# Performance work log

Measured on AMD Instinct MI355X. Metric: run time of the kernel, lower is better.

Reference implementation:

```python
import jax, jax.numpy as jnp
import numpy as np

N, E, F0, H, ED, C = 50000, 800000, 32, 64, 13, 10
EPS_BN = 1e-5
EPS_STD = 1e-5


def setup_inputs() -> dict:
    keys = iter(jax.random.split(jax.random.key(0), 64))

    def w(shape):
        return jax.random.normal(next(keys), shape, jnp.float32) * 0.05

    inp = {
        "x": jax.random.normal(next(keys), (N, F0), jnp.float32),
        "edge_index": jax.random.randint(next(keys), (2, E), 0, N),
        "edge_attr": jax.random.normal(next(keys), (E, ED), jnp.float32),
    }
    for l, (fi, fo) in enumerate([(F0, H), (H, 2 * H), (2 * H, 4 * H)], 1):
        inp[f"we{l}"] = w((ED, fi));   inp[f"be{l}"] = jnp.zeros((fi,), jnp.float32)   # edge encoder
        inp[f"wp{l}"] = w((3 * fi, fi)); inp[f"bp{l}"] = jnp.zeros((fi,), jnp.float32)  # pre-MLP (1 layer)
        inp[f"wo{l}"] = w((13 * fi, fo)); inp[f"bo{l}"] = jnp.zeros((fo,), jnp.float32) # post-MLP (1 layer)
        inp[f"wl{l}"] = w((fo, fo));   inp[f"bl{l}"] = jnp.zeros((fo,), jnp.float32)   # PNAConv.lin
        inp[f"g{l}"] = jnp.ones((fo,), jnp.float32); inp[f"bb{l}"] = jnp.zeros((fo,), jnp.float32)  # BatchNorm
    inp["wc"] = w((4 * H, C)); inp["bc"] = jnp.zeros((C,), jnp.float32)  # classifier
    return inp


def _pna_conv(x, src, dst, edge_attr, cnt, avg_log, we, be, wp, bp, wo, bo, wl, bl):
    n = x.shape[0]
    e = edge_attr @ we + be                            # [E, F_in] edge encoder
    h = jnp.concatenate([x[dst], x[src], e], -1)       # [E, 3*F_in] = (x_i, x_j, edge)
    m = h @ wp + bp                                    # pre-MLP message, [E, F_in]
    denom = jnp.maximum(cnt, 1.0)[:, None]
    mean = jax.ops.segment_sum(m, dst, n) / denom
    mean2 = jax.ops.segment_sum(m * m, dst, n) / denom
    has = (cnt > 0)[:, None]
    mn = jnp.where(has, jax.ops.segment_min(m, dst, n), 0.0)
    mx = jnp.where(has, jax.ops.segment_max(m, dst, n), 0.0)
    std = jnp.sqrt(jax.nn.relu(mean2 - mean * mean) + EPS_STD)
    agg = jnp.concatenate([mean, mn, mx, std], -1)     # [N, 4*F_in]
    logd = jnp.log(jnp.maximum(cnt, 1.0) + 1.0)[:, None]
    scaled = jnp.concatenate([agg, agg * (logd / avg_log), agg * (avg_log / logd)], -1)  # [N, 12*F_in]
    out = jnp.concatenate([x, scaled], -1) @ wo + bo   # post-MLP on [N, 13*F_in]
    return out @ wl + bl                                # PNAConv.lin


def _bn_relu(x, g, b):
    mu = jnp.mean(x, 0)
    var = jnp.mean((x - mu) ** 2, 0)  # biased, training-mode BatchNorm
    return jax.nn.relu(g * (x - mu) / jnp.sqrt(var + EPS_BN) + b)


def _forward(edge_index, x, edge_attr, *p):
    src, dst = edge_index[0], edge_index[1]
    n = x.shape[0]
    cnt = jax.ops.segment_sum(jnp.ones((edge_index.shape[1],), jnp.float32), dst, n)
    avg_log = jnp.mean(jnp.log(cnt + 1.0))  # PNA avg_deg['log'] from in-degree histogram
    (we1, be1, wp1, bp1, wo1, bo1, wl1, bl1, g1, bb1,
     we2, be2, wp2, bp2, wo2, bo2, wl2, bl2, g2, bb2,
     we3, be3, wp3, bp3, wo3, bo3, wl3, bl3, g3, bb3, wc, bc) = p
    x = _bn_relu(_pna_conv(x, src, dst, edge_attr, cnt, avg_log, we1, be1, wp1, bp1, wo1, bo1, wl1, bl1), g1, bb1)
    x = _bn_relu(_pna_conv(x, src, dst, edge_attr, cnt, avg_log, we2, be2, wp2, bp2, wo2, bo2, wl2, bl2), g2, bb2)
    x = _bn_relu(_pna_conv(x, src, dst, edge_attr, cnt, avg_log, we3, be3, wp3, bp3, wo3, bo3, wl3, bl3), g3, bb3)
    return x @ wc + bc


def reference(x, edge_index, edge_attr,
              we1, be1, wp1, bp1, wo1, bo1, wl1, bl1, g1, bb1,
              we2, be2, wp2, bp2, wo2, bo2, wl2, bl2, g2, bb2,
              we3, be3, wp3, bp3, wo3, bo3, wl3, bl3, g3, bb3,
              wc, bc):
    return _forward(edge_index, x, edge_attr,
                    we1, be1, wp1, bp1, wo1, bo1, wl1, bl1, g1, bb1,
                    we2, be2, wp2, bp2, wo2, bo2, wl2, bl2, g2, bb2,
                    we3, be3, wp3, bp3, wo3, bo3, wl3, bl3, g3, bb3, wc, bc)
```

## Files before the change

### kernel.cpp

```cpp
#include <hip/hip_runtime.h>
#include <math.h>
#include <float.h>

#define NN 50000
#define NE 800000

typedef __attribute__((ext_vector_type(8))) short bf16x8;
typedef __attribute__((ext_vector_type(4))) short bf16x4;
typedef __attribute__((ext_vector_type(2))) short bf16x2;
typedef __attribute__((ext_vector_type(4))) float f32x4;

template<int NC> struct VecT;
template<> struct VecT<2>{ using type = bf16x2; };
template<> struct VecT<4>{ using type = bf16x4; };

__device__ inline short f2bf(float f){
  union { float f; unsigned u; } v; v.f = f;
  unsigned u = v.u + 0x7FFFu + ((v.u >> 16) & 1u);
  return (short)(u >> 16);
}

__device__ inline float bf2f(short b){
  union { unsigned u; float f; } v;
  v.u = ((unsigned)(unsigned short)b) << 16;
  return v.f;
}


__global__ void k_count(const int* __restrict__ dst, int* __restrict__ cnt){
  int e = blockIdx.x*blockDim.x + threadIdx.x;
  if (e < NE) atomicAdd(&cnt[dst[e]], 1);
}

__global__ void k_scan_part(const int* __restrict__ cnt, int* __restrict__ offs, int* __restrict__ totals){
  __shared__ int sh[1024];
  int t = threadIdx.x, i = blockIdx.x*1024 + t;
  int v = (i < NN) ? cnt[i] : 0;
  sh[t] = v; __syncthreads();
  for (int off = 1; off < 1024; off <<= 1){
    int x = (t >= off) ? sh[t-off] : 0;
    __syncthreads();
    sh[t] += x;
    __syncthreads();
  }
  if (i < NN) offs[i] = sh[t] - v;
  if (t == 1023) totals[blockIdx.x] = sh[t];
}

__global__ void k_scan_tops(int* totals, int nb){
  if (threadIdx.x == 0){
    int acc = 0;
    for (int i = 0; i < nb; i++){ int v = totals[i]; totals[i] = acc; acc += v; }
  }
}

__global__ void k_scan_add(int* __restrict__ offs, const int* __restrict__ totals, int* __restrict__ cursor){
  int i = blockIdx.x*blockDim.x + threadIdx.x;
  if (i < NN){
    int v = offs[i] + totals[i >> 10];
    offs[i] = v;
    cursor[i] = v;
  } else if (i == NN){
    offs[NN] = NE;
  }
}

__global__ void k_scatter(const int* __restrict__ ei, int* __restrict__ cursor,
                          int* __restrict__ ssrc, int* __restrict__ seid){
  int e = blockIdx.x*blockDim.x + threadIdx.x;
  if (e >= NE) return;
  int d = ei[NE + e];
  int p = atomicAdd(&cursor[d], 1);
  ssrc[p] = ei[e];
  seid[p] = e;
}

__global__ void k_permute_ea(const float* __restrict__ ea, const int* __restrict__ seid,
                             short* __restrict__ ea_s){
  int i = blockIdx.x*blockDim.x + threadIdx.x;
  if (i >= NE*16) return;
  int p = i >> 4, r = i & 15;
  int eid = seid[p];
  float v = (r < 13) ? ea[(size_t)eid*13 + r] : ((r == 13) ? 1.0f : 0.f);
  ea_s[i] = f2bf(v);
}

__global__ void k_sumlog(const int* __restrict__ cnt, float* __restrict__ sumlog){
  __shared__ float sh[256];
  int t = threadIdx.x;
  float s = 0.f;
  for (int i = blockIdx.x*256 + t; i < NN; i += gridDim.x*256)
    s += logf((float)cnt[i] + 1.f);
  sh[t] = s; __syncthreads();
  for (int o = 128; o > 0; o >>= 1){ if (t < o) sh[t] += sh[t+o]; __syncthreads(); }
  if (t == 0) atomicAdd(sumlog, sh[0]);
}

__global__ void k_rscale(const int* __restrict__ cnt, const float* __restrict__ sumlog,
                         float* __restrict__ r1, float* __restrict__ r2){
  int i = blockIdx.x*blockDim.x + threadIdx.x;
  if (i >= NN) return;
  float avg = sumlog[0] / (float)NN;
  float logd = logf(fmaxf((float)cnt[i], 1.f) + 1.f);
  r1[i] = logd / avg;
  r2[i] = avg / logd;
}

__global__ void k_f2bf_arr(const float* __restrict__ in, short* __restrict__ out, int n){
  int i = blockIdx.x*blockDim.x + threadIdx.x;
  if (i < n) out[i] = f2bf(in[i]);
}

__global__ void k_prep_wcT(const float* __restrict__ wc, short* __restrict__ wcT){
  int idx = blockIdx.x*blockDim.x + threadIdx.x;
  if (idx >= 2560) return;
  int c = idx >> 8, k = idx & 255;
  wcT[idx] = f2bf(wc[k*10 + c]);
}

__global__ __launch_bounds__(256) void k_prep_wol(int K13, int fo,
    const float* __restrict__ wo, const float* __restrict__ wl,
    short* __restrict__ WolT)
{
  __shared__ short As[64*40];
  __shared__ short Bs[64*40];
  int tid = threadIdx.x;
  int lane = tid & 63, w = tid >> 6;
  int wr = w >> 1, wc = w & 1;
  int l15 = lane & 15, l16 = lane >> 4;
  int row0 = blockIdx.x*64, col0 = blockIdx.y*64;
  int sr = tid >> 2, sq = tid & 3;
  f32x4 acc[2][2] = {};
  for (int k0 = 0; k0 < fo; k0 += 32){
    int gr = row0 + sr;
    bf16x8 av = {0,0,0,0,0,0,0,0};
    if (gr < K13){
      const float4* src = (const float4*)(wo + (size_t)gr*fo + k0 + sq*8);
      float4 f0 = src[0], f1 = src[1];
      av[0]=f2bf(f0.x); av[1]=f2bf(f0.y); av[2]=f2bf(f0.z); av[3]=f2bf(f0.w);
      av[4]=f2bf(f1.x); av[5]=f2bf(f1.y); av[6]=f2bf(f1.z); av[7]=f2bf(f1.w);
    }
    *(bf16x8*)&As[sr*40 + sq*8] = av;
    int gc = col0 + sr;
    bf16x8 bv;
    #pragma unroll
    for (int e = 0; e < 8; e++)
      bv[e] = f2bf(wl[(size_t)(k0 + sq*8 + e)*fo + gc]);
    *(bf16x8*)&Bs[sr*40 + sq*8] = bv;
    __syncthreads();
    bf16x8 af[2], bg[2];
    #pragma unroll
    for (int m = 0; m < 2; m++) af[m] = *(bf16x8*)&As[(wr*32 + m*16 + l15)*40 + l16*8];
    #pragma unroll
    for (int n = 0; n < 2; n++) bg[n] = *(bf16x8*)&Bs[(wc*32 + n*16 + l15)*40 + l16*8];
    #pragma unroll
    for (int m = 0; m < 2; m++)
      #pragma unroll
      for (int n = 0; n < 2; n++)
        acc[m][n] = __builtin_amdgcn_mfma_f32_16x16x32_bf16(af[m], bg[n], acc[m][n], 0, 0, 0);
    __syncthreads();
  }
  #pragma unroll
  for (int m = 0; m < 2; m++){
    #pragma unroll
    for (int n = 0; n < 2; n++){
      int gcol = col0 + wc*32 + n*16 + l15;
      int grow0 = row0 + wr*32 + m*16 + l16*4;
      if (grow0 < K13){
        bf16x4 ov;
        #pragma unroll
        for (int i = 0; i < 4; i++) ov[i] = f2bf(acc[m][n][i]);
        *(bf16x4*)(WolT + (size_t)gcol*K13 + grow0) = ov;
      }
    }
  }
}

__global__ void k_prep_layer(const float* __restrict__ we, const float* __restrict__ be,
                             const float* __restrict__ wp, const float* __restrict__ bp,
                             short* __restrict__ WeLT, float* __restrict__ bL2,
                             short* __restrict__ wpT,
                             float* __restrict__ bns, int fi, int NCW){
  int fo = 2*fi;
  int n0 = fi*32;
  int n1 = n0 + 2*fi;
  int n2 = n1 + 2*fi*fi;
  int n3 = n2 + 2*fo;
  int idx = blockIdx.x*blockDim.x + threadIdx.x;
  if (idx < n0){
    int jg = idx >> 5, k = idx & 31;
    int Wd = NCW*16;
    int sub = jg / Wd, j = jg - sub*Wd;
    int f = sub*Wd + NCW*(j & 15) + (j >> 4);
    float s = 0.f;
    if (k < 13){
      const float* wpb = wp + (size_t)2*fi*fi;
      const float* wr = we + k*fi;
      for (int jj = 0; jj < fi; jj++) s += wr[jj] * wpb[(size_t)jj*fi + f];
    }
    WeLT[idx] = f2bf(s);
  } else if (idx < n1){
    int f = idx - n0;
    if (f >= fi){ bL2[f] = 0.f; }
    else {
      const float* wpb = wp + (size_t)2*fi*fi;
      float s = bp[f];
      for (int j = 0; j < fi; j++) s += be[j] * wpb[(size_t)j*fi + f];
      bL2[f] = s;
    }
  } else if (idx < n2){
    int id = idx - n1;
    int s = id/(fi*fi), rem = id - s*fi*fi;
    int f = rem/fi, j = rem - f*fi;
    wpT[id] = f2bf(wp[((size_t)s*fi + j)*fi + f]);
  } else if (idx < n3){
    bns[idx - n2] = 0.f;
  }
}

__global__ __launch_bounds__(256) void k_gemm_t(int M, int Nout, int K,
    const short* __restrict__ A, const short* __restrict__ BT,
    const float* __restrict__ bias, short* __restrict__ Cb)
{
  __shared__ short As[64*40];
  __shared__ short Bs[64*40];
  int tid = threadIdx.x;
  int lane = tid & 63, w = tid >> 6;
  int wr = w >> 1, wc = w & 1;
  int l15 = lane & 15, l16 = lane >> 4;
  int row0 = blockIdx.x*64, col0 = blockIdx.y*64;
  int sr = tid >> 2, sq = tid & 3;
  f32x4 acc[2][2] = {};
  for (int k0 = 0; k0 < K; k0 += 32){
    int gr = row0 + sr;
    bf16x8 av = {0,0,0,0,0,0,0,0};
    if (gr < M) av = *(const bf16x8*)(A + (size_t)gr*K + k0 + sq*8);
    *(bf16x8*)&As[sr*40 + sq*8] = av;
    int gc = col0 + sr;
    bf16x8 bv = {0,0,0,0,0,0,0,0};
    if (gc < Nout) bv = *(const bf16x8*)(BT + (size_t)gc*K + k0 + sq*8);
    *(bf16x8*)&Bs[sr*40 + sq*8] = bv;
    __syncthreads();
    bf16x8 af[2], bg[2];
    #pragma unroll
    for (int m = 0; m < 2; m++) af[m] = *(bf16x8*)&As[(wr*32 + m*16 + l15)*40 + l16*8];
    #pragma unroll
    for (int n = 0; n < 2; n++) bg[n] = *(bf16x8*)&Bs[(wc*32 + n*16 + l15)*40 + l16*8];
    #pragma unroll
    for (int m = 0; m < 2; m++)
      #pragma unroll
      for (int n = 0; n < 2; n++)
        acc[m][n] = __builtin_amdgcn_mfma_f32_16x16x32_bf16(af[m], bg[n], acc[m][n], 0, 0, 0);
    __syncthreads();
  }
  #pragma unroll
  for (int m = 0; m < 2; m++){
    #pragma unroll
    for (int n = 0; n < 2; n++){
      int gcol = col0 + wc*32 + n*16 + l15;
      #pragma unroll
      for (int i = 0; i < 4; i++){
        int grow = row0 + wr*32 + m*16 + l16*4 + i;
        if (grow < M && gcol < Nout)
          Cb[(size_t)grow*Nout + gcol] = f2bf(acc[m][n][i] + (bias ? bias[gcol] : 0.f));
      }
    }
  }
}

__global__ __launch_bounds__(256) void k_mfma(int M, int Nout, int K,
    const short* __restrict__ A,
    const short* __restrict__ BT, int ldbt,
    float* __restrict__ C, int ldc, const float* __restrict__ bias)
{
  __shared__ short As[64*40];
  __shared__ short Bs[64*40];
  int tid = threadIdx.x;
  int lane = tid & 63, w = tid >> 6;
  int wr = w >> 1, wc = w & 1;
  int l15 = lane & 15, l16 = lane >> 4;
  int row0 = blockIdx.x*64, col0 = blockIdx.y*64;
  int sr = tid >> 2, sq = tid & 3;
  f32x4 acc[2][2] = {};
  for (int k0 = 0; k0 < K; k0 += 32){
    int gr = row0 + sr;
    bf16x8 av = {0,0,0,0,0,0,0,0};
    if (gr < M) av = *(const bf16x8*)(A + (size_t)gr*K + k0 + sq*8);
    *(bf16x8*)&As[sr*40 + sq*8] = av;
    int gc = col0 + sr;
    bf16x8 bv = {0,0,0,0,0,0,0,0};
    if (gc < Nout)
      bv = *(const bf16x8*)(BT + (size_t)gc*ldbt + k0 + sq*8);
    *(bf16x8*)&Bs[sr*40 + sq*8] = bv;
    __syncthreads();
    bf16x8 af[2], bg[2];
    #pragma unroll
    for (int m = 0; m < 2; m++) af[m] = *(bf16x8*)&As[(wr*32 + m*16 + l15)*40 + l16*8];
    #pragma unroll
    for (int n = 0; n < 2; n++) bg[n] = *(bf16x8*)&Bs[(wc*32 + n*16 + l15)*40 + l16*8];
    #pragma unroll
    for (int m = 0; m < 2; m++)
      #pragma unroll
      for (int n = 0; n < 2; n++)
        acc[m][n] = __builtin_amdgcn_mfma_f32_16x16x32_bf16(af[m], bg[n], acc[m][n], 0, 0, 0);
    __syncthreads();
  }
  #pragma unroll
  for (int m = 0; m < 2; m++){
    #pragma unroll
    for (int n = 0; n < 2; n++){
      int gcol = col0 + wc*32 + n*16 + l15;
      #pragma unroll
      for (int i = 0; i < 4; i++){
        int grow = row0 + wr*32 + m*16 + l16*4 + i;
        if (grow < M && gcol < Nout)
          C[(size_t)grow*ldc + gcol] = acc[m][n][i] + (bias ? bias[gcol] : 0.f);
      }
    }
  }
}

template<int MREP, int WCG>
__global__ __launch_bounds__(512) void k_mfma_big(int M, int K, int FI,
    const short* __restrict__ P0, const short* __restrict__ P1,
    const short* __restrict__ P2, const short* __restrict__ P3,
    const short* __restrict__ P4,
    const float* __restrict__ r1, const float* __restrict__ r2,
    const short* __restrict__ BT,
    short* __restrict__ Cb, float* __restrict__ bns)
{
  constexpr int NOUT = WCG*64;
  constexpr int ROWS = (8/WCG)*MREP*16;
  constexpr int NR = 8/WCG;
  __shared__ short As[2][ROWS*40];
  __shared__ short Bs[2][NOUT*40];
  const short* Pt[5] = {P0, P1, P2, P3, P4};
  int tid = threadIdx.x;
  int lane = tid & 63, w = tid >> 6;
  int wid_c = w % WCG, wid_r = w / WCG;
  int wrow = wid_r * (MREP*16);
  int wcol = wid_c * 64;
  int l15 = lane & 15, l16 = lane >> 4;
  int row0 = blockIdx.x*ROWS;
  int trowA = tid >> 2, tsegA = tid & 3;
  int trowB = tid >> 1, tsegB = tid & 1;
  int gr = row0 + trowA;
  bool aval = gr < M;
  bool bval = trowB < NOUT;
  const short* bsrc = BT + (size_t)trowB*K + tsegB*16;
  f32x4 acc[MREP][4] = {};
  int nt = K/32;

  bf16x8 a0 = {0,0,0,0,0,0,0,0}, b0 = a0, b1 = a0;
  float sval = 1.f; int smv = 0;

  auto LOAD = [&](int t){
    int k0 = t*32;
    int kb = k0 / FI;
    int pi = (kb == 0) ? 0 : ((kb - 1) & 3) + 1;
    smv = (kb == 0) ? 0 : ((kb - 1) >> 2);
    const short* __restrict__ P = Pt[pi];
    int j0 = k0 - kb*FI + tsegA*8;
    bf16x8 z = {0,0,0,0,0,0,0,0};
    a0 = z; b0 = z; b1 = z;
    sval = 1.f;
    if (aval){
      a0 = *(const bf16x8*)(P + (size_t)gr*FI + j0);
      if (smv) sval = (smv == 1) ? r1[gr] : r2[gr];
    }
    if (bval){
      const bf16x8* src = (const bf16x8*)(bsrc + k0);
      b0 = src[0]; b1 = src[1];
    }
  };

  LOAD(0);
  int cur = 0;
  for (int t = 0; t < nt; t++){
    if (smv && aval){
      #pragma unroll
      for (int e = 0; e < 8; e++) a0[e] = f2bf(bf2f(a0[e])*sval);
    }
    *(bf16x8*)&As[cur][trowA*40 + tsegA*8] = a0;
    if (bval){
      *(bf16x8*)&Bs[cur][trowB*40 + tsegB*16]     = b0;
      *(bf16x8*)&Bs[cur][trowB*40 + tsegB*16 + 8] = b1;
    }
    __syncthreads();
    if (t + 1 < nt) LOAD(t + 1);
    bf16x8 af[MREP], bg[4];
    #pragma unroll
    for (int m = 0; m < MREP; m++) af[m] = *(bf16x8*)&As[cur][(wrow + m*16 + l15)*40 + l16*8];
    #pragma unroll
    for (int n = 0; n < 4; n++) bg[n] = *(bf16x8*)&Bs[cur][(wcol + n*16 + l15)*40 + l16*8];
    #pragma unroll
    for (int m = 0; m < MREP; m++)
      #pragma unroll
      for (int n = 0; n < 4; n++)
        acc[m][n] = __builtin_amdgcn_mfma_f32_16x16x32_bf16(af[m], bg[n], acc[m][n], 0, 0, 0);
    cur ^= 1;
  }
  float ws[4], ws2[4];
  #pragma unroll
  for (int n = 0; n < 4; n++){
    int gcol = wcol + n*16 + l15;
    float s = 0.f, s2 = 0.f;
    #pragma unroll
    for (int m = 0; m < MREP; m++)
      #pragma unroll
      for (int i = 0; i < 4; i++){
        float v = acc[m][n][i];
        s += v; s2 = fmaf(v, v, s2);
        int grow = row0 + wrow + m*16 + l16*4 + i;
        if (grow < M) Cb[(size_t)grow*NOUT + gcol] = f2bf(v);
      }
    s  += __shfl_xor(s, 16, 64);  s  += __shfl_xor(s, 32, 64);
    s2 += __shfl_xor(s2, 16, 64); s2 += __shfl_xor(s2, 32, 64);
    ws[n] = s; ws2[n] = s2;
  }
  float* red = (float*)&As[0][0];
  __syncthreads();
  if (l16 == 0){
    #pragma unroll
    for (int n = 0; n < 4; n++){
      red[w*128 + n*16 + l15]      = ws[n];
      red[w*128 + 64 + n*16 + l15] = ws2[n];
    }
  }
  __syncthreads();
  if (wid_r == 0 && l16 == 0){
    #pragma unroll
    for (int n = 0; n < 4; n++){
      float ts = 0.f, ts2 = 0.f;
      #pragma unroll
      for (int r = 0; r < NR; r++){
        int ww = r*WCG + wid_c;
        ts  += red[ww*128 + n*16 + l15];
        ts2 += red[ww*128 + 64 + n*16 + l15];
      }
      int gcol = wcol + n*16 + l15;
      atomicAdd(&bns[gcol], ts);
      atomicAdd(&bns[NOUT + gcol], ts2);
    }
  }
}

template<int NC, int FI>
__global__ __launch_bounds__(256) void k_agg3(
    const int* __restrict__ offs, const int* __restrict__ ssrc,
    const short* __restrict__ ea_s,
    const short* __restrict__ T,
    const short* __restrict__ WeLT,
    short* __restrict__ mean, short* __restrict__ mn,
    short* __restrict__ mx,  short* __restrict__ stdv)
{
  constexpr int SUBS = FI / (NC*16);
  constexpr int STR = 2*FI;
  using bf16xN = typename VecT<NC>::type;
  const short* t_s = T + FI;
  int wv = (blockIdx.x*blockDim.x + threadIdx.x) >> 6;
  int n = wv / SUBS, sub = wv - n*SUBS;
  if (n >= NN) return;
  int lane = threadIdx.x & 63;
  int l15 = lane & 15, l16 = lane >> 4;
  int c0 = sub * NC * 16;
  bool ins = (l16 == 1);
  bf16xN tdv = *(const bf16xN*)(T + (size_t)n*STR + c0 + NC*l15);
  bf16x8 bfrag[NC];
  #pragma unroll
  for (int c = 0; c < NC; c++){
    bfrag[c] = *(const bf16x8*)(WeLT + (size_t)(c0 + c*16 + l15)*32 + l16*8);
    if (ins) bfrag[c][5] = tdv[c];
  }
  float s[NC], s2[NC], vmn[NC], vmx[NC];
  #pragma unroll
  for (int c = 0; c < NC; c++){ s[c]=0.f; s2[c]=0.f; vmn[c]=FLT_MAX; vmx[c]=-FLT_MAX; }
  int e0 = offs[n], e1 = offs[n+1];
  int p0 = e0;
  int tsoff = c0 + NC*l15;
  for (; p0 + 16 <= e1; p0 += 16){
    bf16x8 afrag = *(const bf16x8*)(ea_s + (size_t)(p0 + l15)*16 + l16*8);
    bf16xN tsv[4];
    #pragma unroll
    for (int i = 0; i < 4; i++){
      int src = ssrc[p0 + l16*4 + i];
      tsv[i] = *(const bf16xN*)(t_s + (size_t)src*STR + tsoff);
    }
    #pragma unroll
    for (int c = 0; c < NC; c++){
      f32x4 acc = {0.f,0.f,0.f,0.f};
      acc = __builtin_amdgcn_mfma_f32_16x16x32_bf16(afrag, bfrag[c], acc, 0, 0, 0);
      #pragma unroll
      for (int i = 0; i < 4; i++){
        float m = acc[i] + bf2f(tsv[i][c]);
        s[c] += m;
        s2[c] = fmaf(m, m, s2[c]);
        vmn[c] = fminf(vmn[c], m);
        vmx[c] = fmaxf(vmx[c], m);
      }
    }
  }
  if (p0 < e1){
    int pa = p0 + l15; if (pa > e1-1) pa = e1-1;
    bf16x8 afrag = *(const bf16x8*)(ea_s + (size_t)pa*16 + l16*8);
    bf16xN tsv[4]; bool val[4];
    #pragma unroll
    for (int i = 0; i < 4; i++){
      int pp = p0 + l16*4 + i;
      val[i] = pp < e1;
      int pc = val[i] ? pp : (e1-1);
      int src = ssrc[pc];
      tsv[i] = *(const bf16xN*)(t_s + (size_t)src*STR + tsoff);
    }
    #pragma unroll
    for (int c = 0; c < NC; c++){
      f32x4 acc = {0.f,0.f,0.f,0.f};
      acc = __builtin_amdgcn_mfma_f32_16x16x32_bf16(afrag, bfrag[c], acc, 0, 0, 0);
      #pragma unroll
      for (int i = 0; i < 4; i++){
        float m = acc[i] + bf2f(tsv[i][c]);
        float mv = val[i] ? m : 0.f;
        s[c] += mv;
        s2[c] = fmaf(mv, mv, s2[c]);
        vmn[c] = fminf(vmn[c], val[i] ? m :  FLT_MAX);
        vmx[c] = fmaxf(vmx[c], val[i] ? m : -FLT_MAX);
      }
    }
  }
  int cdeg = e1 - e0;
  float denom = fmaxf((float)cdeg, 1.f);
  float rden = 1.0f / denom;
  short* outp = (l16==0) ? mean : (l16==1) ? mn : (l16==2) ? mx : stdv;
  bf16xN ov;
  #pragma unroll
  for (int c = 0; c < NC; c++){
    float sv = s[c];   sv  += __shfl_xor(sv, 16, 64);  sv  += __shfl_xor(sv, 32, 64);
    float s2v = s2[c]; s2v += __shfl_xor(s2v, 16, 64); s2v += __shfl_xor(s2v, 32, 64);
    float mnv = vmn[c]; mnv = fminf(mnv, __shfl_xor(mnv, 16, 64)); mnv = fminf(mnv, __shfl_xor(mnv, 32, 64));
    float mxv = vmx[c]; mxv = fmaxf(mxv, __shfl_xor(mxv, 16, 64)); mxv = fmaxf(mxv, __shfl_xor(mxv, 32, 64));
    float me = sv*rden, me2 = s2v*rden;
    float sd = sqrtf(fmaxf(me2 - me*me, 0.f) + 1e-5f);
    float val = (l16==0) ? me : (l16==1) ? (cdeg>0 ? mnv : 0.f)
              : (l16==2) ? (cdeg>0 ? mxv : 0.f) : sd;
    ov[c] = f2bf(val);
  }
  *(bf16xN*)(outp + (size_t)n*FI + c0 + NC*l15) = ov;
}

__global__ void k_bn_apply(const short* __restrict__ x, const float* __restrict__ sums,
                           const float* __restrict__ g, const float* __restrict__ b,
                           short* __restrict__ xbf, int fo, int total){
  int i = blockIdx.x*blockDim.x + threadIdx.x;
  if (i >= total) return;
  int col = i % fo;
  float mu = sums[col] / (float)NN;
  float var = sums[fo + col] / (float)NN - mu*mu;
  float v = (bf2f(x[i]) - mu) * rsqrtf(var + 1e-5f) * g[col] + b[col];
  xbf[i] = f2bf(fmaxf(v, 0.f));
}

extern "C" void kernel_launch(void* const* d_in, const int* in_sizes, int n_in,
                              void* d_out, int out_size, void* d_ws, size_t ws_size,
                              hipStream_t stream){
  const float* x0 = (const float*)d_in[0];
  const int*   ei = (const int*)d_in[1];
  const float* ea = (const float*)d_in[2];
  const float* W[35];
  for (int i = 0; i < 35; i++) W[i] = (const float*)d_in[i];
  const float* wc = W[33];
  const float* bc = W[34];

  char* w = (char*)d_ws;
  auto alloc = [&](size_t bytes)->void*{
    void* p = (void*)w; w += (bytes + 255) & ~(size_t)255; return p;
  };
  int* cnt    = (int*)alloc((size_t)NN*4);
  int* offs   = (int*)alloc((size_t)(NN+1)*4);
  int* cursor = (int*)alloc((size_t)NN*4);
  int* totals = (int*)alloc(64*4);
  int* ssrc   = (int*)alloc((size_t)NE*4);
  int* seid   = (int*)alloc((size_t)NE*4);
  float* sumlog = (float*)alloc(256);
  float* r1   = (float*)alloc((size_t)NN*4);
  float* r2   = (float*)alloc((size_t)NN*4);
  float* bns  = (float*)alloc(512*4);
  float* bL2  = (float*)alloc(256*4);
  short* WeLT = (short*)alloc((size_t)128*32*2);
  short* WolT = (short*)alloc((size_t)256*1664*2);
  short* wpT  = (short*)alloc((size_t)2*128*128*2);
  short* wcT  = (short*)alloc((size_t)10*256*2);
  short* ea_s = (short*)alloc((size_t)(NE+16)*16*2);
  short* agg[4];
  for (int a = 0; a < 4; a++) agg[a] = (short*)alloc((size_t)NN*128*2);
  short* F    = (short*)alloc((size_t)NN*256*2);
  short* xbfA = (short*)alloc((size_t)NN*128*2);
  short* xbfB = (short*)alloc((size_t)NN*256*2);

  hipMemsetAsync(cnt, 0, (size_t)NN*4, stream);
  hipMemsetAsync(sumlog, 0, 4, stream);
  k_count<<<(NE+255)/256, 256, 0, stream>>>(ei + NE, cnt);
  k_scan_part<<<49, 1024, 0, stream>>>(cnt, offs, totals);
  k_scan_tops<<<1, 64, 0, stream>>>(totals, 49);
  k_scan_add<<<(NN+256)/256, 256, 0, stream>>>(offs, totals, cursor);
  k_scatter<<<(NE+255)/256, 256, 0, stream>>>(ei, cursor, ssrc, seid);
  k_permute_ea<<<(NE*16+255)/256, 256, 0, stream>>>(ea, seid, ea_s);
  k_sumlog<<<256, 256, 0, stream>>>(cnt, sumlog);
  k_rscale<<<(NN+255)/256, 256, 0, stream>>>(cnt, sumlog, r1, r2);
  k_prep_wcT<<<10, 256, 0, stream>>>(wc, wcT);
  k_f2bf_arr<<<(NN*32+255)/256, 256, 0, stream>>>(x0, xbfA, NN*32);

  const short* xin = xbfA;
  const int fis[3] = {32, 64, 128};
  const int ncws[3] = {2, 4, 4};
  const int GX = (NN + 63) / 64;
  const int GB2 = (NN + 127) / 128;
  for (int l = 0; l < 3; l++){
    int fi = fis[l], fo = 2*fi;
    const float* we = W[3+10*l+0], *be = W[3+10*l+1];
    const float* wp = W[3+10*l+2], *bp = W[3+10*l+3];
    const float* wo = W[3+10*l+4];
    const float* wl = W[3+10*l+6];
    const float* g  = W[3+10*l+8], *bb = W[3+10*l+9];

    short* T = F;

    int K13 = 13*fi;
    dim3 gw((K13 + 63)/64, fo/64);
    k_prep_wol<<<gw, 256, 0, stream>>>(K13, fo, wo, wl, WolT);

    int nprep = fi*32 + 2*fi + 2*fi*fi + 2*fo;
    k_prep_layer<<<(nprep+255)/256, 256, 0, stream>>>(we, be, wp, bp,
        WeLT, bL2, wpT, bns, fi, ncws[l]);

    dim3 gt(GX, (2*fi) / 64);
    k_gemm_t<<<gt, 256, 0, stream>>>(NN, 2*fi, fi, xin, wpT, bL2, T);

    if (l == 0){
      int GA3 = (NN*64 + 255)/256;
      k_agg3<2,32><<<GA3, 256, 0, stream>>>(offs, ssrc, ea_s, T, WeLT,
          agg[0], agg[1], agg[2], agg[3]);
    } else if (l == 1){
      int GA3 = (NN*64 + 255)/256;
      k_agg3<4,64><<<GA3, 256, 0, stream>>>(offs, ssrc, ea_s, T, WeLT,
          agg[0], agg[1], agg[2], agg[3]);
    } else {
      int GA3 = (NN*2*64 + 255)/256;
      k_agg3<4,128><<<GA3, 256, 0, stream>>>(offs, ssrc, ea_s, T, WeLT,
          agg[0], agg[1], agg[2], agg[3]);
    }

    if (l == 0)
      k_mfma_big<1,1><<<GB2, 512, 0, stream>>>(NN, 13*fi, fi, xin, agg[0], agg[1], agg[2], agg[3],
          r1, r2, WolT, F, bns);
    else if (l == 1)
      k_mfma_big<2,2><<<GB2, 512, 0, stream>>>(NN, 13*fi, fi, xin, agg[0], agg[1], agg[2], agg[3],
          r1, r2, WolT, F, bns);
    else
      k_mfma_big<4,4><<<GB2, 512, 0, stream>>>(NN, 13*fi, fi, xin, agg[0], agg[1], agg[2], agg[3],
          r1, r2, WolT, F, bns);

    short* xbf_next = (l == 0) ? xbfB : ((l == 1) ? xbfA : xbfB);
    k_bn_apply<<<((NN*fo)+255)/256, 256, 0, stream>>>(F, bns, g, bb, xbf_next, fo, NN*fo);

    xin = xbf_next;
  }

  dim3 gc(GX, 1);
  k_mfma<<<gc, 256, 0, stream>>>(NN, 10, 256, xin, wcT, 256, (float*)d_out, 10, bc);
}
```

Before: 605.5 us.

## Fuse BatchNorm+ReLU into next layer's GEMM operand loads and vectorize edge-attr permute

Removes the standalone BN-apply pass by computing per-channel scale/shift coefficients in a tiny kernel and applying BN+ReLU on the fly when the next layer's GEMMs (and the classifier) load their A operand. Ping-pong F buffers replace the separate bf16 activation buffers. The edge-attribute permute now handles one edge per thread with vectorized 16-byte stores, and the aggregation drops redundant min/max masking. The cost is that BN is recomputed in several consumer kernels (gemm_t, mfma_big x-segment, classifier), which adds ALU work and extra loads of bnc to each of them.

```diff
diff --git a/kernel.cpp b/kernel.cpp
--- a/kernel.cpp
+++ b/kernel.cpp
@@ -77,12 +77,18 @@
 
 __global__ void k_permute_ea(const float* __restrict__ ea, const int* __restrict__ seid,
                              short* __restrict__ ea_s){
-  int i = blockIdx.x*blockDim.x + threadIdx.x;
-  if (i >= NE*16) return;
-  int p = i >> 4, r = i & 15;
+  int p = blockIdx.x*blockDim.x + threadIdx.x;
+  if (p >= NE) return;
   int eid = seid[p];
-  float v = (r < 13) ? ea[(size_t)eid*13 + r] : ((r == 13) ? 1.0f : 0.f);
-  ea_s[i] = f2bf(v);
+  const float* src = ea + (size_t)eid*13;
+  short out[16];
+  #pragma unroll
+  for (int r = 0; r < 13; r++) out[r] = f2bf(src[r]);
+  out[13] = (short)0x3F80;
+  out[14] = 0; out[15] = 0;
+  bf16x8* dst = (bf16x8*)(ea_s + (size_t)p*16);
+  dst[0] = *(bf16x8*)&out[0];
+  dst[1] = *(bf16x8*)&out[8];
 }
 
 __global__ void k_sumlog(const int* __restrict__ cnt, float* __restrict__ sumlog){
@@ -116,6 +122,17 @@
   if (idx >= 2560) return;
   int c = idx >> 8, k = idx & 255;
   wcT[idx] = f2bf(wc[k*10 + c]);
+}
+
+__global__ void k_bn_coef(const float* __restrict__ bns, const float* __restrict__ g,
+                          const float* __restrict__ b, float* __restrict__ bnc, int fo){
+  int c = threadIdx.x;
+  if (c >= fo) return;
+  float mu = bns[c] / (float)NN;
+  float var = bns[fo + c] / (float)NN - mu*mu;
+  float sc = g[c] * rsqrtf(var + 1e-5f);
+  bnc[c] = sc;
+  bnc[256 + c] = b[c] - mu*sc;
 }
 
 __global__ __launch_bounds__(256) void k_prep_wol(int K13, int fo,
@@ -220,7 +237,8 @@
 
 __global__ __launch_bounds__(256) void k_gemm_t(int M, int Nout, int K,
     const short* __restrict__ A, const short* __restrict__ BT,
-    const float* __restrict__ bias, short* __restrict__ Cb)
+    const float* __restrict__ bias, short* __restrict__ Cb,
+    const float* __restrict__ bnc)
 {
   __shared__ short As[64*40];
   __shared__ short Bs[64*40];
@@ -234,7 +252,17 @@
   for (int k0 = 0; k0 < K; k0 += 32){
     int gr = row0 + sr;
     bf16x8 av = {0,0,0,0,0,0,0,0};
-    if (gr < M) av = *(const bf16x8*)(A + (size_t)gr*K + k0 + sq*8);
+    if (gr < M){
+      av = *(const bf16x8*)(A + (size_t)gr*K + k0 + sq*8);
+      if (bnc){
+        int cb = k0 + sq*8;
+        #pragma unroll
+        for (int e = 0; e < 8; e++){
+          float v = fmaf(bf2f(av[e]), bnc[cb + e], bnc[256 + cb + e]);
+          av[e] = f2bf(fmaxf(v, 0.f));
+        }
+      }
+    }
     *(bf16x8*)&As[sr*40 + sq*8] = av;
     int gc = col0 + sr;
     bf16x8 bv = {0,0,0,0,0,0,0,0};
@@ -271,7 +299,8 @@
 __global__ __launch_bounds__(256) void k_mfma(int M, int Nout, int K,
     const short* __restrict__ A,
     const short* __restrict__ BT, int ldbt,
-    float* __restrict__ C, int ldc, const float* __restrict__ bias)
+    float* __restrict__ C, int ldc, const float* __restrict__ bias,
+    const float* __restrict__ bnc)
 {
   __shared__ short As[64*40];
   __shared__ short Bs[64*40];
@@ -285,7 +314,17 @@
   for (int k0 = 0; k0 < K; k0 += 32){
     int gr = row0 + sr;
     bf16x8 av = {0,0,0,0,0,0,0,0};
-    if (gr < M) av = *(const bf16x8*)(A + (size_t)gr*K + k0 + sq*8);
+    if (gr < M){
+      av = *(const bf16x8*)(A + (size_t)gr*K + k0 + sq*8);
+      if (bnc){
+        int cb = k0 + sq*8;
+        #pragma unroll
+        for (int e = 0; e < 8; e++){
+          float v = fmaf(bf2f(av[e]), bnc[cb + e], bnc[256 + cb + e]);
+          av[e] = f2bf(fmaxf(v, 0.f));
+        }
+      }
+    }
     *(bf16x8*)&As[sr*40 + sq*8] = av;
     int gc = col0 + sr;
     bf16x8 bv = {0,0,0,0,0,0,0,0};
@@ -327,7 +366,8 @@
     const short* __restrict__ P4,
     const float* __restrict__ r1, const float* __restrict__ r2,
     const short* __restrict__ BT,
-    short* __restrict__ Cb, float* __restrict__ bns)
+    short* __restrict__ Cb, float* __restrict__ bns,
+    const float* __restrict__ bnc)
 {
   constexpr int NOUT = WCG*64;
   constexpr int ROWS = (8/WCG)*MREP*16;
@@ -352,13 +392,14 @@
   int nt = K/32;
 
   bf16x8 a0 = {0,0,0,0,0,0,0,0}, b0 = a0, b1 = a0;
-  float sval = 1.f; int smv = 0;
+  float sval = 1.f; int smv = 0; int bnk = 0;
 
   auto LOAD = [&](int t){
     int k0 = t*32;
     int kb = k0 / FI;
     int pi = (kb == 0) ? 0 : ((kb - 1) & 3) + 1;
     smv = (kb == 0) ? 0 : ((kb - 1) >> 2);
+    bnk = (kb == 0) ? 1 : 0;
     const short* __restrict__ P = Pt[pi];
     int j0 = k0 - kb*FI + tsegA*8;
     bf16x8 z = {0,0,0,0,0,0,0,0};
@@ -367,6 +408,13 @@
     if (aval){
       a0 = *(const bf16x8*)(P + (size_t)gr*FI + j0);
       if (smv) sval = (smv == 1) ? r1[gr] : r2[gr];
+      if (bnk && bnc){
+        #pragma unroll
+        for (int e = 0; e < 8; e++){
+          float v = fmaf(bf2f(a0[e]), bnc[j0 + e], bnc[256 + j0 + e]);
+          a0[e] = f2bf(fmaxf(v, 0.f));
+        }
+      }
     }
     if (bval){
       const bf16x8* src = (const bf16x8*)(bsrc + k0);
@@ -509,8 +557,7 @@
       int pp = p0 + l16*4 + i;
       val[i] = pp < e1;
       int pc = val[i] ? pp : (e1-1);
-      int src = ssrc[pc];
-      tsv[i] = *(const bf16xN*)(t_s + (size_t)src*STR + tsoff);
+      tsv[i] = *(const bf16xN*)(t_s + (size_t)ssrc[pc]*STR + tsoff);
     }
     #pragma unroll
     for (int c = 0; c < NC; c++){
@@ -522,8 +569,8 @@
         float mv = val[i] ? m : 0.f;
         s[c] += mv;
         s2[c] = fmaf(mv, mv, s2[c]);
-        vmn[c] = fminf(vmn[c], val[i] ? m :  FLT_MAX);
-        vmx[c] = fmaxf(vmx[c], val[i] ? m : -FLT_MAX);
+        vmn[c] = fminf(vmn[c], m);
+        vmx[c] = fmaxf(vmx[c], m);
       }
     }
   }
@@ -547,18 +594,6 @@
   *(bf16xN*)(outp + (size_t)n*FI + c0 + NC*l15) = ov;
 }
 
-__global__ void k_bn_apply(const short* __restrict__ x, const float* __restrict__ sums,
-                           const float* __restrict__ g, const float* __restrict__ b,
-                           short* __restrict__ xbf, int fo, int total){
-  int i = blockIdx.x*blockDim.x + threadIdx.x;
-  if (i >= total) return;
-  int col = i % fo;
-  float mu = sums[col] / (float)NN;
-  float var = sums[fo + col] / (float)NN - mu*mu;
-  float v = (bf2f(x[i]) - mu) * rsqrtf(var + 1e-5f) * g[col] + b[col];
-  xbf[i] = f2bf(fmaxf(v, 0.f));
-}
-
 extern "C" void kernel_launch(void* const* d_in, const int* in_sizes, int n_in,
                               void* d_out, int out_size, void* d_ws, size_t ws_size,
                               hipStream_t stream){
@@ -584,6 +619,7 @@
   float* r1   = (float*)alloc((size_t)NN*4);
   float* r2   = (float*)alloc((size_t)NN*4);
   float* bns  = (float*)alloc(512*4);
+  float* bnc  = (float*)alloc(3*512*4);
   float* bL2  = (float*)alloc(256*4);
   short* WeLT = (short*)alloc((size_t)128*32*2);
   short* WolT = (short*)alloc((size_t)256*1664*2);
@@ -592,9 +628,9 @@
   short* ea_s = (short*)alloc((size_t)(NE+16)*16*2);
   short* agg[4];
   for (int a = 0; a < 4; a++) agg[a] = (short*)alloc((size_t)NN*128*2);
-  short* F    = (short*)alloc((size_t)NN*256*2);
+  short* FA   = (short*)alloc((size_t)NN*256*2);
+  short* FB   = (short*)alloc((size_t)NN*256*2);
   short* xbfA = (short*)alloc((size_t)NN*128*2);
-  short* xbfB = (short*)alloc((size_t)NN*256*2);
 
   hipMemsetAsync(cnt, 0, (size_t)NN*4, stream);
   hipMemsetAsync(sumlog, 0, 4, stream);
@@ -603,13 +639,14 @@
   k_scan_tops<<<1, 64, 0, stream>>>(totals, 49);
   k_scan_add<<<(NN+256)/256, 256, 0, stream>>>(offs, totals, cursor);
   k_scatter<<<(NE+255)/256, 256, 0, stream>>>(ei, cursor, ssrc, seid);
-  k_permute_ea<<<(NE*16+255)/256, 256, 0, stream>>>(ea, seid, ea_s);
+  k_permute_ea<<<(NE+255)/256, 256, 0, stream>>>(ea, seid, ea_s);
   k_sumlog<<<256, 256, 0, stream>>>(cnt, sumlog);
   k_rscale<<<(NN+255)/256, 256, 0, stream>>>(cnt, sumlog, r1, r2);
   k_prep_wcT<<<10, 256, 0, stream>>>(wc, wcT);
   k_f2bf_arr<<<(NN*32+255)/256, 256, 0, stream>>>(x0, xbfA, NN*32);
 
-  const short* xin = xbfA;
+  const short* act = xbfA;
+  const float* actBN = nullptr;
   const int fis[3] = {32, 64, 128};
   const int ncws[3] = {2, 4, 4};
   const int GX = (NN + 63) / 64;
@@ -622,7 +659,8 @@
     const float* wl = W[3+10*l+6];
     const float* g  = W[3+10*l+8], *bb = W[3+10*l+9];
 
-    short* T = F;
+    short* Fcur = (l & 1) ? FB : FA;
+    short* T = Fcur;
 
     int K13 = 13*fi;
     dim3 gw((K13 + 63)/64, fo/64);
@@ -633,7 +671,7 @@
         WeLT, bL2, wpT, bns, fi, ncws[l]);
 
     dim3 gt(GX, (2*fi) / 64);
-    k_gemm_t<<<gt, 256, 0, stream>>>(NN, 2*fi, fi, xin, wpT, bL2, T);
+    k_gemm_t<<<gt, 256, 0, stream>>>(NN, 2*fi, fi, act, wpT, bL2, T, actBN);
 
     if (l == 0){
       int GA3 = (NN*64 + 255)/256;
@@ -650,21 +688,21 @@
     }
 
     if (l == 0)
-      k_mfma_big<1,1><<<GB2, 512, 0, stream>>>(NN, 13*fi, fi, xin, agg[0], agg[1], agg[2], agg[3],
-          r1, r2, WolT, F, bns);
+      k_mfma_big<1,1><<<GB2, 512, 0, stream>>>(NN, 13*fi, fi, act, agg[0], agg[1], agg[2], agg[3],
+          r1, r2, WolT, Fcur, bns, actBN);
     else if (l == 1)
-      k_mfma_big<2,2><<<GB2, 512, 0, stream>>>(NN, 13*fi, fi, xin, agg[0], agg[1], agg[2], agg[3],
-          r1, r2, WolT, F, bns);
+      k_mfma_big<2,2><<<GB2, 512, 0, stream>>>(NN, 13*fi, fi, act, agg[0], agg[1], agg[2], agg[3],
+          r1, r2, WolT, Fcur, bns, actBN);
     else
-      k_mfma_big<4,4><<<GB2, 512, 0, stream>>>(NN, 13*fi, fi, xin, agg[0], agg[1], agg[2], agg[3],
-          r1, r2, WolT, F, bns);
-
-    short* xbf_next = (l == 0) ? xbfB : ((l == 1) ? xbfA : xbfB);
-    k_bn_apply<<<((NN*fo)+255)/256, 256, 0, stream>>>(F, bns, g, bb, xbf_next, fo, NN*fo);
-
-    xin = xbf_next;
+      k_mfma_big<4,4><<<GB2, 512, 0, stream>>>(NN, 13*fi, fi, act, agg[0], agg[1], agg[2], agg[3],
+          r1, r2, WolT, Fcur, bns, actBN);
+
+    k_bn_coef<<<1, 256, 0, stream>>>(bns, g, bb, bnc + l*512, fo);
+
+    act = Fcur;
+    actBN = bnc + l*512;
   }
 
   dim3 gc(GX, 1);
-  k_mfma<<<gc, 256, 0, stream>>>(NN, 10, 256, xin, wcT, 256, (float*)d_out, 10, bc);
-}
+  k_mfma<<<gc, 256, 0, stream>>>(NN, 10, 256, act, wcT, 256, (float*)d_out, 10, bc, actBN);
+}
```

Result: faster. 563.9 us (-6.9%).
